# Kernel tuning notes

Hardware: AMD Instinct MI355X
Metric: run time of the kernel (lower is better)

## Reference

```python
import jax, jax.numpy as jnp
import numpy as np

D_MODEL = 512
D_STATE = 64
D_INNER = 2 * D_MODEL   # standard Mamba expand=2
D_CONV = 4
DT_RANK = D_MODEL // 16  # 32
LN_EPS = 1e-5


def setup_inputs() -> dict:
    key = jax.random.key(0)
    ks = jax.random.split(key, 12)
    B, L = 2, 1024
    s = 0.02
    return {
        "frames": jax.random.normal(ks[0], (B, L, D_MODEL), jnp.float32),
        "gamma": jnp.ones((D_MODEL,), jnp.float32),
        "beta": jnp.zeros((D_MODEL,), jnp.float32),
        "W_in": jax.random.normal(ks[1], (D_MODEL, 2 * D_INNER), jnp.float32) * s,
        "conv_w": jax.random.normal(ks[2], (D_INNER, D_CONV), jnp.float32) * s,
        "conv_b": jnp.zeros((D_INNER,), jnp.float32),
        "W_x": jax.random.normal(ks[3], (D_INNER, DT_RANK + 2 * D_STATE), jnp.float32) * s,
        "W_dt": jax.random.normal(ks[4], (DT_RANK, D_INNER), jnp.float32) * s,
        "b_dt": jax.random.uniform(ks[5], (D_INNER,), jnp.float32, -4.0, -2.0),
        "A_log": jnp.log(jnp.broadcast_to(jnp.arange(1, D_STATE + 1, dtype=jnp.float32), (D_INNER, D_STATE))),
        "D": jnp.ones((D_INNER,), jnp.float32),
        "W_out": jax.random.normal(ks[6], (D_INNER, D_MODEL), jnp.float32) * s,
    }


def reference(frames, gamma, beta, W_in, conv_w, conv_b, W_x, W_dt, b_dt, A_log, D, W_out):
    B, L, _ = frames.shape
    d_inner = W_in.shape[1] // 2
    d_state = A_log.shape[1]
    dt_rank = W_dt.shape[0]
    d_conv = conv_w.shape[1]

    # LayerNorm
    mu = frames.mean(-1, keepdims=True)
    var = ((frames - mu) ** 2).mean(-1, keepdims=True)
    xn = (frames - mu) * jax.lax.rsqrt(var + LN_EPS) * gamma + beta

    # in_proj -> x, z
    x, z = jnp.split(xn @ W_in, 2, axis=-1)  # each (B, L, d_inner)

    # causal depthwise conv1d along time
    xc = jnp.pad(x.transpose(0, 2, 1), ((0, 0), (0, 0), (d_conv - 1, 0)))  # (B, d_inner, L+pad)
    xconv = jax.lax.conv_general_dilated(
        xc, conv_w[:, None, :], (1,), "VALID", feature_group_count=d_inner)  # (B, d_inner, L)
    x = jax.nn.silu(xconv.transpose(0, 2, 1) + conv_b)  # (B, L, d_inner)

    # input-dependent dt, B, C
    xdb = x @ W_x
    dt, Bm, Cm = jnp.split(xdb, [dt_rank, dt_rank + d_state], axis=-1)
    delta = jax.nn.softplus(dt @ W_dt + b_dt)  # (B, L, d_inner)
    A = -jnp.exp(A_log)                        # (d_inner, d_state)

    # selective scan over time
    def step(h, inp):
        d_t, B_t, C_t, x_t = inp  # (B,d_inner) (B,d_state) (B,d_state) (B,d_inner)
        dA = jnp.exp(d_t[..., None] * A)                       # (B,d_inner,d_state)
        h = h * dA + (d_t * x_t)[..., None] * B_t[:, None, :]  # (B,d_inner,d_state)
        y = jnp.einsum("bds,bs->bd", h, C_t)
        return h, y

    h0 = jnp.zeros((B, d_inner, d_state), frames.dtype)
    xs = (delta.transpose(1, 0, 2), Bm.transpose(1, 0, 2),
          Cm.transpose(1, 0, 2), x.transpose(1, 0, 2))
    _, ys = jax.lax.scan(step, h0, xs)  # (L, B, d_inner)

    y = ys.transpose(1, 0, 2) + x * D
    y = y * jax.nn.silu(z)
    return y @ W_out + frames  # residual connection
```

## Files before the change

kernel.cpp:

```cpp
#include <hip/hip_runtime.h>
#include <hip/hip_bf16.h>
#include <math.h>

constexpr int Bn     = 2;
constexpr int Lseq   = 1024;
constexpr int DM     = 512;
constexpr int DI     = 1024;
constexpr int DS     = 64;
constexpr int RNK    = 32;
constexpr int NROWS  = Bn * Lseq;
constexpr int XDBW   = RNK + 2 * DS;
constexpr int CH     = 64;
constexpr int NC     = Lseq / CH;
constexpr int DROWS  = 8;

constexpr float LOG2E = 1.44269504088896340736f;

typedef __attribute__((ext_vector_type(4))) float floatx4;
typedef __attribute__((ext_vector_type(8))) short shortx8;

__device__ __forceinline__ float silu_f(float v) {
    return v / (1.f + __expf(-v));
}

__device__ __forceinline__ float rdl(float v, int l) {
    return __int_as_float(__builtin_amdgcn_readlane(__float_as_int(v), l));
}

__device__ __forceinline__ float bf2f(unsigned short u) {
    return __uint_as_float((unsigned)u << 16);
}

__device__ __forceinline__ float exp2_fast(float x) {
#if __has_builtin(__builtin_amdgcn_exp2f)
    return __builtin_amdgcn_exp2f(x);
#else
    return exp2f(x);
#endif
}

__global__ void prep_kernel(const float* __restrict__ x, const float* __restrict__ g,
                            const float* __restrict__ be,
                            const float* __restrict__ Wi, const float* __restrict__ Wo,
                            const float* __restrict__ Wx,
                            __hip_bfloat16* __restrict__ xn,
                            __hip_bfloat16* __restrict__ Ti, __hip_bfloat16* __restrict__ To,
                            __hip_bfloat16* __restrict__ Tx) {
    __shared__ float tile[64][65];
    __shared__ float red[8];
    int bid = blockIdx.x;
    int tid = threadIdx.x;
    if (bid < NROWS) {
        int row = bid;
        const float* xr = x + (size_t)row * DM;
        float v0 = xr[tid], v1 = xr[tid + 256];
        float s = v0 + v1, sq = v0 * v0 + v1 * v1;
        #pragma unroll
        for (int o = 1; o < 64; o <<= 1) {
            s  += __shfl_xor(s, o);
            sq += __shfl_xor(sq, o);
        }
        int w = tid >> 6;
        if ((tid & 63) == 0) { red[w] = s; red[4 + w] = sq; }
        __syncthreads();
        float ts = red[0] + red[1] + red[2] + red[3];
        float tq = red[4] + red[5] + red[6] + red[7];
        float mu  = ts * (1.f / DM);
        float var = tq * (1.f / DM) - mu * mu;
        float inv = rsqrtf(var + 1e-5f);
        __hip_bfloat16* o0 = xn + (size_t)row * DM;
        o0[tid]       = __float2bfloat16((v0 - mu) * inv * g[tid]       + be[tid]);
        o0[tid + 256] = __float2bfloat16((v1 - mu) * inv * g[tid + 256] + be[tid + 256]);
        return;
    }
    int b2 = bid - NROWS;
    const float* in; __hip_bfloat16* out; int R, Cc, bx, by;
    if (b2 < 256)      { in = Wi; out = Ti; R = DM; Cc = 2 * DI; bx = b2 & 31; by = b2 >> 5; }
    else if (b2 < 384) { int b3 = b2 - 256; in = Wo; out = To; R = DI; Cc = DM;   bx = b3 & 7; by = b3 >> 3; }
    else               { int b3 = b2 - 384; in = Wx; out = Tx; R = DI; Cc = XDBW; bx = b3 % 3; by = b3 / 3; }
    int r0 = by * 64, c0 = bx * 64;
    #pragma unroll
    for (int i = tid; i < 4096; i += 256) {
        int r = i >> 6, c = i & 63;
        tile[r][c] = (r0 + r < R && c0 + c < Cc) ? in[(size_t)(r0 + r) * Cc + c0 + c] : 0.f;
    }
    __syncthreads();
    #pragma unroll
    for (int i = tid; i < 4096; i += 256) {
        int c = i >> 6, r = i & 63;
        if (r0 + r < R && c0 + c < Cc)
            out[(size_t)(c0 + c) * R + r0 + r] = __float2bfloat16(tile[r][c]);
    }
}

__global__ __launch_bounds__(512) void gemm_inproj(const __hip_bfloat16* __restrict__ A,
                                                   const __hip_bfloat16* __restrict__ Bt,
                                                   __hip_bfloat16* __restrict__ xh,
                                                   __hip_bfloat16* __restrict__ zh,
                                                   int M, int N, int K) {
    __shared__ __hip_bfloat16 As[128 * 64];
    __shared__ __hip_bfloat16 Bs[128 * 64];
    const int tid  = threadIdx.x;
    const int wave = tid >> 6, lane = tid & 63;
    const int m0 = blockIdx.y * 128, n0 = blockIdx.x * 128;
    const int wm = (wave >> 2) * 64, wn = (wave & 3) * 32;

    floatx4 acc[4][2] = {};

    const int arow16 = lane & 15;
    const int kgrp   = lane >> 4;

    for (int k0 = 0; k0 < K; k0 += 64) {
        #pragma unroll
        for (int p = 0; p < 2; ++p) {
            int j = tid + p * 512;
            int h = j >> 9, rs = j & 511;
            int row = rs >> 2, seg = rs & 3;
            const __hip_bfloat16* gA = A  + (size_t)(m0 + row) * K + k0 + h * 32 + seg * 8;
            const __hip_bfloat16* gB = Bt + (size_t)(n0 + row) * K + k0 + h * 32 + seg * 8;
            __hip_bfloat16* lA = As + (size_t)(wave * 64 + p * 512) * 8;
            __hip_bfloat16* lB = Bs + (size_t)(wave * 64 + p * 512) * 8;
            __builtin_amdgcn_global_load_lds(
                (const __attribute__((address_space(1))) void*)gA,
                (__attribute__((address_space(3))) void*)lA, 16, 0, 0);
            __builtin_amdgcn_global_load_lds(
                (const __attribute__((address_space(1))) void*)gB,
                (__attribute__((address_space(3))) void*)lB, 16, 0, 0);
        }
        __syncthreads();

        const shortx8* Asv = (const shortx8*)As;
        const shortx8* Bsv = (const shortx8*)Bs;
        #pragma unroll
        for (int h = 0; h < 2; ++h) {
            shortx8 a[4], b[2];
            #pragma unroll
            for (int i = 0; i < 4; ++i)
                a[i] = Asv[h * 512 + (wm + i * 16 + arow16) * 4 + kgrp];
            #pragma unroll
            for (int j = 0; j < 2; ++j)
                b[j] = Bsv[h * 512 + (wn + j * 16 + arow16) * 4 + kgrp];
            #pragma unroll
            for (int i = 0; i < 4; ++i)
                #pragma unroll
                for (int j = 0; j < 2; ++j)
                    acc[i][j] = __builtin_amdgcn_mfma_f32_16x16x32_bf16(a[i], b[j], acc[i][j], 0, 0, 0);
        }
        __syncthreads();
    }

    const int drow = (lane >> 4) * 4;
    const int dcol = lane & 15;
    const bool isz = (n0 >= DI);
    __hip_bfloat16* dst = isz ? zh : xh;
    const int coloff = isz ? DI : 0;
    #pragma unroll
    for (int i = 0; i < 4; ++i)
        #pragma unroll
        for (int j = 0; j < 2; ++j) {
            int rowb = m0 + wm + i * 16 + drow;
            int col  = n0 + wn + j * 16 + dcol - coloff;
            #pragma unroll
            for (int r = 0; r < 4; ++r)
                dst[(size_t)(rowb + r) * DI + col] = __float2bfloat16(acc[i][j][r]);
        }
}

template<bool RES>
__global__ __launch_bounds__(512) void gemm64_sk(const __hip_bfloat16* __restrict__ A,
                                                 const __hip_bfloat16* __restrict__ Bt,
                                                 const float* __restrict__ Res,
                                                 float* __restrict__ C,
                                                 int M, int N, int K) {
    __shared__ __hip_bfloat16 As[2][64 * 64];
    __shared__ __hip_bfloat16 Bs[2][64 * 64];
    __shared__ float red[256 * 17];
    const int tid  = threadIdx.x;
    const int wave = tid >> 6, lane = tid & 63;
    const int g = wave >> 2, w2 = wave & 3;
    const int m0 = blockIdx.y * 64, n0 = blockIdx.x * 64;
    const int wm = (w2 >> 1) * 32, wn = (w2 & 1) * 32;

    floatx4 acc[2][2] = {};

    const int arow16 = lane & 15;
    const int kgrp   = lane >> 4;
    const int kbeg   = g * (K / 2);

    for (int kk = 0; kk < K / 2; kk += 64) {
        int k0 = kbeg + kk;
        #pragma unroll
        for (int p = 0; p < 2; ++p) {
            int j = (w2 * 64 + lane) + p * 256;
            int h = j >> 8, rs = j & 255;
            int row = rs >> 2, seg = rs & 3;
            int brow = n0 + row; if (brow >= N) brow = N - 1;
            const __hip_bfloat16* gA = A  + (size_t)(m0 + row) * K + k0 + h * 32 + seg * 8;
            const __hip_bfloat16* gB = Bt + (size_t)brow * K + k0 + h * 32 + seg * 8;
            __hip_bfloat16* lA = As[g] + (size_t)(w2 * 64 + p * 256) * 8;
            __hip_bfloat16* lB = Bs[g] + (size_t)(w2 * 64 + p * 256) * 8;
            __builtin_amdgcn_global_load_lds(
                (const __attribute__((address_space(1))) void*)gA,
                (__attribute__((address_space(3))) void*)lA, 16, 0, 0);
            __builtin_amdgcn_global_load_lds(
                (const __attribute__((address_space(1))) void*)gB,
                (__attribute__((address_space(3))) void*)lB, 16, 0, 0);
        }
        __syncthreads();

        const shortx8* Asv = (const shortx8*)As[g];
        const shortx8* Bsv = (const shortx8*)Bs[g];
        #pragma unroll
        for (int h = 0; h < 2; ++h) {
            shortx8 a[2], b[2];
            #pragma unroll
            for (int i = 0; i < 2; ++i)
                a[i] = Asv[h * 256 + (wm + i * 16 + arow16) * 4 + kgrp];
            #pragma unroll
            for (int j = 0; j < 2; ++j)
                b[j] = Bsv[h * 256 + (wn + j * 16 + arow16) * 4 + kgrp];
            #pragma unroll
            for (int i = 0; i < 2; ++i)
                #pragma unroll
                for (int j = 0; j < 2; ++j)
                    acc[i][j] = __builtin_amdgcn_mfma_f32_16x16x32_bf16(a[i], b[j], acc[i][j], 0, 0, 0);
        }
        __syncthreads();
    }

    int rbase = (w2 * 64 + lane) * 17;
    if (g == 1) {
        #pragma unroll
        for (int i = 0; i < 2; ++i)
            #pragma unroll
            for (int j = 0; j < 2; ++j)
                *(float4*)&red[rbase + (i * 2 + j) * 4] =
                    make_float4(acc[i][j][0], acc[i][j][1], acc[i][j][2], acc[i][j][3]);
    }
    __syncthreads();
    if (g == 0) {
        const int drow = (lane >> 4) * 4;
        const int dcol = lane & 15;
        #pragma unroll
        for (int i = 0; i < 2; ++i)
            #pragma unroll
            for (int j = 0; j < 2; ++j) {
                float4 part = *(const float4*)&red[rbase + (i * 2 + j) * 4];
                int rowb = m0 + wm + i * 16 + drow;
                int col  = n0 + wn + j * 16 + dcol;
                if (col < N) {
                    #pragma unroll
                    for (int r = 0; r < 4; ++r) {
                        size_t idx = (size_t)(rowb + r) * N + col;
                        float v = acc[i][j][r] + (&part.x)[r];
                        if (RES) v += Res[idx];
                        C[idx] = v;
                    }
                }
            }
    }
}

__global__ __launch_bounds__(256) void conv_tile(const __hip_bfloat16* __restrict__ xh,
                                                 const __hip_bfloat16* __restrict__ zh,
                                                 const float* __restrict__ cw,
                                                 const float* __restrict__ cb,
                                                 __hip_bfloat16* __restrict__ xcv_bf,
                                                 __hip_bfloat16* __restrict__ xcvT,
                                                 __hip_bfloat16* __restrict__ zgT) {
    __shared__ float xt[67][68];
    __shared__ float tb[64][65];
    __shared__ float tb2[64][65];
    int t0 = blockIdx.x * 64, d0 = blockIdx.y * 64, b = blockIdx.z;
    int tid = threadIdx.x;
    size_t rowbase = (size_t)b * Lseq;

    for (int i = tid; i < 67 * 16; i += 256) {
        int r = i >> 4, j = i & 15;
        int t = t0 - 3 + r;
        float4 v4 = make_float4(0.f, 0.f, 0.f, 0.f);
        if (t >= 0) {
            ushort4 u = *(const ushort4*)&xh[(rowbase + t) * DI + d0 + j * 4];
            v4 = make_float4(bf2f(u.x), bf2f(u.y), bf2f(u.z), bf2f(u.w));
        }
        *(float4*)&xt[r][j * 4] = v4;
    }
    for (int i = tid; i < 64 * 16; i += 256) {
        int r = i >> 4, j = i & 15;
        ushort4 u = *(const ushort4*)&zh[(rowbase + t0 + r) * DI + d0 + j * 4];
        tb2[r][j * 4 + 0] = silu_f(bf2f(u.x));
        tb2[r][j * 4 + 1] = silu_f(bf2f(u.y));
        tb2[r][j * 4 + 2] = silu_f(bf2f(u.z));
        tb2[r][j * 4 + 3] = silu_f(bf2f(u.w));
    }
    __syncthreads();

    {
        int d = tid & 63, tg = tid >> 6;
        float4 cwv = *(const float4*)&cw[(d0 + d) * 4];
        float cbv = cb[d0 + d];
        #pragma unroll
        for (int i = 0; i < 16; ++i) {
            int t = tg * 16 + i;
            float acc = cbv;
            #pragma unroll
            for (int k = 0; k < 4; ++k) acc += xt[t + k][d] * (&cwv.x)[k];
            float v = silu_f(acc);
            tb[t][d] = v;
            xcv_bf[(rowbase + t0 + t) * DI + d0 + d] = __float2bfloat16(v);
        }
    }
    __syncthreads();

    {
        int t2 = tid & 63, dg2 = tid >> 6;
        #pragma unroll
        for (int i = 0; i < 16; ++i) {
            int d = dg2 * 16 + i;
            size_t orow = ((size_t)(b * DI + d0 + d)) * Lseq + t0 + t2;
            xcvT[orow] = __float2bfloat16(tb[t2][d]);
            zgT[orow]  = __float2bfloat16(tb2[t2][d]);
        }
    }
}

__global__ __launch_bounds__(256) void delta_kernel(const float* __restrict__ xdb,
                                                    const float* __restrict__ Wdt,
                                                    const float* __restrict__ bdt,
                                                    float* __restrict__ delta) {
    int r0 = blockIdx.y * DROWS;
    int d = blockIdx.x * 256 + threadIdx.x;
    __shared__ float dtv[RNK][DROWS];
    if (threadIdx.x < DROWS * RNK) {
        int k = threadIdx.x >> 5, r = threadIdx.x & 31;
        dtv[r][k] = xdb[(size_t)(r0 + k) * XDBW + r];
    }
    __syncthreads();
    float bb = bdt[d];
    float acc[DROWS];
    #pragma unroll
    for (int k = 0; k < DROWS; ++k) acc[k] = bb;
    #pragma unroll
    for (int r = 0; r < RNK; ++r) {
        float wv = Wdt[(size_t)r * DI + d];
        float4 lo = *(const float4*)&dtv[r][0];
        float4 hi = *(const float4*)&dtv[r][4];
        acc[0] += lo.x * wv; acc[1] += lo.y * wv;
        acc[2] += lo.z * wv; acc[3] += lo.w * wv;
        acc[4] += hi.x * wv; acc[5] += hi.y * wv;
        acc[6] += hi.z * wv; acc[7] += hi.w * wv;
    }
    #pragma unroll
    for (int k = 0; k < DROWS; ++k) {
        float a = acc[k];
        float sp = (a > 20.f) ? a : log1pf(__expf(a));
        delta[(size_t)(r0 + k) * DI + d] = sp;
    }
}

__global__ __launch_bounds__(512) void scan_full(
        const float* __restrict__ delta, const __hip_bfloat16* __restrict__ xcvT,
        const float* __restrict__ xdb, const __hip_bfloat16* __restrict__ zgT,
        const float* __restrict__ A_log, const float* __restrict__ Dp,
        __hip_bfloat16* __restrict__ y_row) {
    __shared__ float2 BC[2][64][65];
    __shared__ float dsh[2][64][9];
    __shared__ float P[8][8 * 65];
    __shared__ float T[64 * 9];

    int blk = blockIdx.x;
    int dg  = blk & 127;
    int b   = blk >> 7;
    int tid = threadIdx.x, w = tid >> 6, lane = tid & 63;
    int d = dg * 8 + w;

    float a2 = -__expf(A_log[d * DS + lane]) * LOG2E;
    float Dv = Dp[d];

    const int st_t = tid >> 3, st_d = tid & 7;

    {
        int r0 = b * Lseq;
        #pragma unroll
        for (int k = 0; k < 2; ++k) {
            int i = tid + k * 512;
            int t = i >> 4, sg = i & 15;
            const float* rowp = &xdb[(size_t)(r0 + t) * XDBW + RNK];
            float4 bv = *(const float4*)&rowp[sg * 4];
            float4 cv = *(const float4*)&rowp[DS + sg * 4];
            #pragma unroll
            for (int j = 0; j < 4; ++j)
                BC[0][t][sg * 4 + j] = make_float2((&bv.x)[j], (&cv.x)[j]);
        }
        dsh[0][st_t][st_d] = delta[(size_t)(r0 + st_t) * DI + dg * 8 + st_d];
    }
    __syncthreads();

    const unsigned short* xT = (const unsigned short*)xcvT;
    const unsigned short* zT = (const unsigned short*)zgT;
    const size_t chbase = (size_t)(b * DI + d) * Lseq;

    float xv = bf2f(xT[chbase + lane]);
    float zv = bf2f(zT[chbase + lane]);

    float h = 0.f;
    float* Pw = P[w];
    const int tr = lane & 7, q = lane >> 3;
    const int rdbase = tr * 65 + q * 8;

    for (int c = 0; c < NC; ++c) {
        int cur = c & 1;

        float4 pb0, pc0, pb1, pc1;
        float pd = 0.f, nxv = 0.f, nzv = 0.f;
        if (c + 1 < NC) {
            int r1 = b * Lseq + (c + 1) * CH;
            {
                int t = tid >> 4, sg = tid & 15;
                const float* rowp = &xdb[(size_t)(r1 + t) * XDBW + RNK];
                pb0 = *(const float4*)&rowp[sg * 4];
                pc0 = *(const float4*)&rowp[DS + sg * 4];
            }
            {
                int i = tid + 512;
                int t = i >> 4, sg = i & 15;
                const float* rowp = &xdb[(size_t)(r1 + t) * XDBW + RNK];
                pb1 = *(const float4*)&rowp[sg * 4];
                pc1 = *(const float4*)&rowp[DS + sg * 4];
            }
            pd  = delta[(size_t)(r1 + st_t) * DI + dg * 8 + st_d];
            nxv = bf2f(xT[chbase + (c + 1) * CH + lane]);
            nzv = bf2f(zT[chbase + (c + 1) * CH + lane]);
        }

        int r0 = b * Lseq + c * CH;
        float vd  = dsh[cur][lane][w];
        float vpx = vd * xv;
        float y = 0.f;

        #pragma unroll
        for (int t8 = 0; t8 < 8; ++t8) {
            #pragma unroll
            for (int tt = 0; tt < 8; ++tt) {
                int t = t8 * 8 + tt;
                float2 bc = BC[cur][t][lane];
                h = h * exp2_fast(rdl(vd, t) * a2) + rdl(vpx, t) * bc.x;
                Pw[tt * 65 + lane] = h * bc.y;
            }
            float sacc = 0.f;
            #pragma unroll
            for (int j = 0; j < 8; ++j) sacc += Pw[rdbase + j];
            sacc += __shfl_xor(sacc, 8);
            sacc += __shfl_xor(sacc, 16);
            sacc += __shfl_xor(sacc, 32);
            if (q == t8) y = sacc;
        }

        float yv = (y + xv * Dv) * zv;

        __syncthreads();
        T[lane * 9 + w] = yv;
        if (c + 1 < NC) {
            int nxt = cur ^ 1;
            {
                int t = tid >> 4, sg = tid & 15;
                #pragma unroll
                for (int j = 0; j < 4; ++j)
                    BC[nxt][t][sg * 4 + j] = make_float2((&pb0.x)[j], (&pc0.x)[j]);
            }
            {
                int i = tid + 512;
                int t = i >> 4, sg = i & 15;
                #pragma unroll
                for (int j = 0; j < 4; ++j)
                    BC[nxt][t][sg * 4 + j] = make_float2((&pb1.x)[j], (&pc1.x)[j]);
            }
            dsh[nxt][st_t][st_d] = pd;
        }
        __syncthreads();

        {
            float v = T[st_t * 9 + st_d];
            y_row[(size_t)(r0 + st_t) * DI + dg * 8 + st_d] = __float2bfloat16(v);
        }

        xv = nxv; zv = nzv;
    }
}

extern "C" void kernel_launch(void* const* d_in, const int* in_sizes, int n_in,
                              void* d_out, int out_size, void* d_ws, size_t ws_size,
                              hipStream_t stream) {
    const float* frames = (const float*)d_in[0];
    const float* gamma  = (const float*)d_in[1];
    const float* beta   = (const float*)d_in[2];
    const float* W_in   = (const float*)d_in[3];
    const float* conv_w = (const float*)d_in[4];
    const float* conv_b = (const float*)d_in[5];
    const float* W_x    = (const float*)d_in[6];
    const float* W_dt   = (const float*)d_in[7];
    const float* b_dt   = (const float*)d_in[8];
    const float* A_log  = (const float*)d_in[9];
    const float* Dp     = (const float*)d_in[10];
    const float* W_out  = (const float*)d_in[11];
    float* out = (float*)d_out;

    char* ws = (char*)d_ws;
    __hip_bfloat16* xn_bf  = (__hip_bfloat16*)ws; ws += (size_t)NROWS * DM * 2;
    __hip_bfloat16* Wt_in  = (__hip_bfloat16*)ws; ws += (size_t)(2 * DI) * DM * 2;
    __hip_bfloat16* Wt_out = (__hip_bfloat16*)ws; ws += (size_t)DM * DI * 2;
    __hip_bfloat16* Wt_x   = (__hip_bfloat16*)ws; ws += (size_t)XDBW * DI * 2;
    __hip_bfloat16* y_row  = (__hip_bfloat16*)ws; ws += (size_t)NROWS * DI * 2;
    __hip_bfloat16* xcv_bf = (__hip_bfloat16*)ws; ws += (size_t)NROWS * DI * 2;
    __hip_bfloat16* xh     = (__hip_bfloat16*)ws; ws += (size_t)NROWS * DI * 2;
    __hip_bfloat16* zh     = (__hip_bfloat16*)ws; ws += (size_t)NROWS * DI * 2;
    __hip_bfloat16* xcvT   = (__hip_bfloat16*)ws; ws += (size_t)NROWS * DI * 2;
    __hip_bfloat16* zgT    = (__hip_bfloat16*)ws; ws += (size_t)NROWS * DI * 2;
    float* xdb    = (float*)ws;  ws += (size_t)NROWS * XDBW * 4;
    float* delta  = (float*)ws;  ws += (size_t)NROWS * DI * 4;

    prep_kernel<<<NROWS + 432, 256, 0, stream>>>(frames, gamma, beta, W_in, W_out, W_x,
                                                 xn_bf, Wt_in, Wt_out, Wt_x);

    gemm_inproj<<<dim3(2 * DI / 128, NROWS / 128), 512, 0, stream>>>(
        xn_bf, Wt_in, xh, zh, NROWS, 2 * DI, DM);

    conv_tile<<<dim3(Lseq / 64, DI / 64, Bn), 256, 0, stream>>>(
        xh, zh, conv_w, conv_b, xcv_bf, xcvT, zgT);

    gemm64_sk<false><<<dim3((XDBW + 63) / 64, NROWS / 64), 512, 0, stream>>>(
        xcv_bf, Wt_x, nullptr, xdb, NROWS, XDBW, DI);

    delta_kernel<<<dim3(DI / 256, NROWS / DROWS), 256, 0, stream>>>(xdb, W_dt, b_dt, delta);

    scan_full<<<Bn * (DI / 8), 512, 0, stream>>>(delta, xcvT, xdb, zgT, A_log, Dp, y_row);

    gemm64_sk<true><<<dim3(DM / 64, NROWS / 64), 512, 0, stream>>>(
        y_row, Wt_out, frames, out, NROWS, DM, DI);
}
```

Baseline: 223.3 us.

## Stream scan B/C coefficients directly into registers instead of shared-memory staging

```diff
diff --git a/kernel.cpp b/kernel.cpp
--- a/kernel.cpp
+++ b/kernel.cpp
@@ -363,7 +363,6 @@
         const float* __restrict__ xdb, const __hip_bfloat16* __restrict__ zgT,
         const float* __restrict__ A_log, const float* __restrict__ Dp,
         __hip_bfloat16* __restrict__ y_row) {
-    __shared__ float2 BC[2][64][65];
     __shared__ float dsh[2][64][9];
     __shared__ float P[8][8 * 65];
     __shared__ float T[64 * 9];
@@ -379,21 +378,7 @@
 
     const int st_t = tid >> 3, st_d = tid & 7;
 
-    {
-        int r0 = b * Lseq;
-        #pragma unroll
-        for (int k = 0; k < 2; ++k) {
-            int i = tid + k * 512;
-            int t = i >> 4, sg = i & 15;
-            const float* rowp = &xdb[(size_t)(r0 + t) * XDBW + RNK];
-            float4 bv = *(const float4*)&rowp[sg * 4];
-            float4 cv = *(const float4*)&rowp[DS + sg * 4];
-            #pragma unroll
-            for (int j = 0; j < 4; ++j)
-                BC[0][t][sg * 4 + j] = make_float2((&bv.x)[j], (&cv.x)[j]);
-        }
-        dsh[0][st_t][st_d] = delta[(size_t)(r0 + st_t) * DI + dg * 8 + st_d];
-    }
+    dsh[0][st_t][st_d] = delta[(size_t)(b * Lseq + st_t) * DI + dg * 8 + st_d];
     __syncthreads();
 
     const unsigned short* xT = (const unsigned short*)xcvT;
@@ -408,75 +393,77 @@
     const int tr = lane & 7, q = lane >> 3;
     const int rdbase = tr * 65 + q * 8;
 
+    const float* Bcol = xdb + RNK + lane;
+    const float* Ccol = xdb + RNK + DS + lane;
+
+    float bA[16], cA[16], bB[16], cB[16];
+    #pragma unroll
+    for (int k = 0; k < 16; ++k) {
+        bA[k] = Bcol[(size_t)(b * Lseq + k) * XDBW];
+        cA[k] = Ccol[(size_t)(b * Lseq + k) * XDBW];
+    }
+
     for (int c = 0; c < NC; ++c) {
         int cur = c & 1;
 
-        float4 pb0, pc0, pb1, pc1;
         float pd = 0.f, nxv = 0.f, nzv = 0.f;
         if (c + 1 < NC) {
             int r1 = b * Lseq + (c + 1) * CH;
-            {
-                int t = tid >> 4, sg = tid & 15;
-                const float* rowp = &xdb[(size_t)(r1 + t) * XDBW + RNK];
-                pb0 = *(const float4*)&rowp[sg * 4];
-                pc0 = *(const float4*)&rowp[DS + sg * 4];
-            }
-            {
-                int i = tid + 512;
-                int t = i >> 4, sg = i & 15;
-                const float* rowp = &xdb[(size_t)(r1 + t) * XDBW + RNK];
-                pb1 = *(const float4*)&rowp[sg * 4];
-                pc1 = *(const float4*)&rowp[DS + sg * 4];
-            }
             pd  = delta[(size_t)(r1 + st_t) * DI + dg * 8 + st_d];
             nxv = bf2f(xT[chbase + (c + 1) * CH + lane]);
             nzv = bf2f(zT[chbase + (c + 1) * CH + lane]);
         }
 
         int r0 = b * Lseq + c * CH;
+        int rnext = (c + 1 < NC) ? (r0 + CH) : r0;
+
         float vd  = dsh[cur][lane][w];
         float vpx = vd * xv;
         float y = 0.f;
 
         #pragma unroll
-        for (int t8 = 0; t8 < 8; ++t8) {
-            #pragma unroll
-            for (int tt = 0; tt < 8; ++tt) {
-                int t = t8 * 8 + tt;
-                float2 bc = BC[cur][t][lane];
-                h = h * exp2_fast(rdl(vd, t) * a2) + rdl(vpx, t) * bc.x;
-                Pw[tt * 65 + lane] = h * bc.y;
+        for (int g4 = 0; g4 < 4; ++g4) {
+            int rg = (g4 < 3) ? (r0 + (g4 + 1) * 16) : rnext;
+            if ((g4 & 1) == 0) {
+                #pragma unroll
+                for (int k = 0; k < 16; ++k) {
+                    bB[k] = Bcol[(size_t)(rg + k) * XDBW];
+                    cB[k] = Ccol[(size_t)(rg + k) * XDBW];
+                }
+            } else {
+                #pragma unroll
+                for (int k = 0; k < 16; ++k) {
+                    bA[k] = Bcol[(size_t)(rg + k) * XDBW];
+                    cA[k] = Ccol[(size_t)(rg + k) * XDBW];
+                }
             }
-            float sacc = 0.f;
-            #pragma unroll
-            for (int j = 0; j < 8; ++j) sacc += Pw[rdbase + j];
-            sacc += __shfl_xor(sacc, 8);
-            sacc += __shfl_xor(sacc, 16);
-            sacc += __shfl_xor(sacc, 32);
-            if (q == t8) y = sacc;
+            #pragma unroll
+            for (int half = 0; half < 2; ++half) {
+                #pragma unroll
+                for (int kk = 0; kk < 8; ++kk) {
+                    int k = half * 8 + kk;
+                    int t = g4 * 16 + k;
+                    float Bv = ((g4 & 1) == 0) ? bA[k] : bB[k];
+                    float Cv = ((g4 & 1) == 0) ? cA[k] : cB[k];
+                    h = h * exp2_fast(rdl(vd, t) * a2) + rdl(vpx, t) * Bv;
+                    Pw[kk * 65 + lane] = h * Cv;
+                }
+                float sacc = 0.f;
+                #pragma unroll
+                for (int j = 0; j < 8; ++j) sacc += Pw[rdbase + j];
+                sacc += __shfl_xor(sacc, 8);
+                sacc += __shfl_xor(sacc, 16);
+                sacc += __shfl_xor(sacc, 32);
+                int t8 = g4 * 2 + half;
+                if (q == t8) y = sacc;
+            }
         }
 
         float yv = (y + xv * Dv) * zv;
 
         __syncthreads();
         T[lane * 9 + w] = yv;
-        if (c + 1 < NC) {
-            int nxt = cur ^ 1;
-            {
-                int t = tid >> 4, sg = tid & 15;
-                #pragma unroll
-                for (int j = 0; j < 4; ++j)
-                    BC[nxt][t][sg * 4 + j] = make_float2((&pb0.x)[j], (&pc0.x)[j]);
-            }
-            {
-                int i = tid + 512;
-                int t = i >> 4, sg = i & 15;
-                #pragma unroll
-                for (int j = 0; j < 4; ++j)
-                    BC[nxt][t][sg * 4 + j] = make_float2((&pb1.x)[j], (&pc1.x)[j]);
-            }
-            dsh[nxt][st_t][st_d] = pd;
-        }
+        if (c + 1 < NC) dsh[cur ^ 1][st_t][st_d] = pd;
         __syncthreads();
 
         {
```

Measured after the change: 220.2 us. No clear change (-1.4%).
